# Optimization experiments

Measured on AMD Instinct MI355X. Metric: run time of the kernel, lower is better.

The kernel has to match this reference:

```python
import jax, jax.numpy as jnp
import numpy as np

KERNEL_SIZE = 3  # init kwarg
METRIC = 'MSE'   # init kwarg


def setup_inputs() -> dict:
    key = jax.random.key(0)
    k1, k2, k3 = jax.random.split(key, 3)
    B, H, W, S = 16, 2048, 2048, 5000
    predictions = jax.random.normal(k1, (B, 1, H, W), dtype=jnp.float32)
    # pos[...,0] = px in [0,W), pos[...,1] = py in [0,H)
    station_positions = jax.random.randint(k2, (B, S, 2), 0, 2048, dtype=jnp.int32)
    station_runoffs = jax.random.normal(k3, (B, S), dtype=jnp.float32)
    return {
        'predictions': predictions,
        'station_positions': station_positions,
        'station_runoffs': station_runoffs,
    }


def reference(predictions, station_positions, station_runoffs):
    B, _, H, W = predictions.shape
    kh = KERNEL_SIZE // 2
    # kernel offsets, flattened to (K2,)
    offs = jnp.arange(-kh, kh + 1)
    dy, dx = jnp.meshgrid(offs, offs, indexing='ij')
    dy = dy.reshape(-1)
    dx = dx.reshape(-1)
    px = station_positions[..., 0]  # (B,S) -> width index
    py = station_positions[..., 1]  # (B,S) -> height index
    ys = py[..., None] + dy  # (B,S,K2)
    xs = px[..., None] + dx  # (B,S,K2)
    valid = (ys >= 0) & (ys < H) & (xs >= 0) & (xs < W)
    ysc = jnp.clip(ys, 0, H - 1)
    xsc = jnp.clip(xs, 0, W - 1)
    b_idx = jnp.arange(B)[:, None, None]
    vals = predictions[b_idx, 0, ysc, xsc]  # (B,S,K2) gathered neighborhoods
    validf = valid.astype(predictions.dtype)
    counts = validf.sum(-1)  # >=4 always (corner of 3x3 window)
    avg_pred = (vals * validf).sum(-1) / counts  # (B,S) per-station window mean
    if METRIC == 'MSE':
        per_station = (avg_pred - station_runoffs) ** 2
    else:  # MAE
        per_station = jnp.abs(avg_pred - station_runoffs)
    # original: sum of per-station losses / num_stations
    return jnp.mean(per_station)
```

## Files before the change

### kernel.cpp

```cpp
#include <hip/hip_runtime.h>


#define BB 16
#define HH 2048
#define WW 2048
#define SS 5000
#define NSTATIONS (BB * SS)

__global__ __launch_bounds__(256) void station_loss_kernel(
    const float* __restrict__ pred,
    const int2*  __restrict__ pos,
    const float* __restrict__ runoff,
    float* __restrict__ out)
{
    int t = blockIdx.x * blockDim.x + threadIdx.x;
    float contrib = 0.0f;
    if (t < NSTATIONS) {
        int b = t / SS;
        int2 p = pos[t];
        int px = p.x;
        int py = p.y;
        const float* img = pred + (size_t)b * (size_t)HH * (size_t)WW;

        float sum = 0.0f;
        float cnt = 0.0f;
        #pragma unroll
        for (int dy = -1; dy <= 1; ++dy) {
            int y = py + dy;
            if (y < 0 || y >= HH) continue;
            const float* row = img + (size_t)y * WW;
            #pragma unroll
            for (int dx = -1; dx <= 1; ++dx) {
                int x = px + dx;
                if (x < 0 || x >= WW) continue;
                sum += row[x];
                cnt += 1.0f;
            }
        }
        float avg = sum / cnt;
        float d = avg - runoff[t];
        contrib = d * d * (1.0f / (float)NSTATIONS);
    }

    #pragma unroll
    for (int off = 32; off > 0; off >>= 1)
        contrib += __shfl_down(contrib, off, 64);

    if ((threadIdx.x & 63) == 0)
        atomicAdd(out, contrib);
}

extern "C" void kernel_launch(void* const* d_in, const int* in_sizes, int n_in,
                              void* d_out, int out_size, void* d_ws, size_t ws_size,
                              hipStream_t stream) {
    const float* pred   = (const float*)d_in[0];
    const int2*  pos    = (const int2*)d_in[1];
    const float* runoff = (const float*)d_in[2];
    float* out = (float*)d_out;

    hipMemsetAsync(out, 0, sizeof(float), stream);

    const int threads = 256;
    const int blocks = (NSTATIONS + threads - 1) / threads;
    station_loss_kernel<<<blocks, threads, 0, stream>>>(pred, pos, runoff, out);
}
```

Measured before the change: 319.4 us.

## Replace global atomics with two-stage block-partial reduction and branchless gathers

Each block now reduces its station losses through shared memory and writes one partial to workspace. A single-block second kernel sums the partials and applies the mean scaling, which replaces the memset and per-wave atomicAdd. The window gathers now use clamped indices and masks instead of branches, so all nine loads are issued unconditionally. The cost is an extra kernel launch and a reliance on the workspace buffer.

```diff
diff --git a/kernel.cpp b/kernel.cpp
--- a/kernel.cpp
+++ b/kernel.cpp
@@ -6,12 +6,14 @@
 #define WW 2048
 #define SS 5000
 #define NSTATIONS (BB * SS)
+#define THREADS 256
+#define NBLOCKS ((NSTATIONS + THREADS - 1) / THREADS)
 
-__global__ __launch_bounds__(256) void station_loss_kernel(
+__global__ __launch_bounds__(THREADS) void station_partial_kernel(
     const float* __restrict__ pred,
     const int2*  __restrict__ pos,
     const float* __restrict__ runoff,
-    float* __restrict__ out)
+    float* __restrict__ partials)
 {
     int t = blockIdx.x * blockDim.x + threadIdx.x;
     float contrib = 0.0f;
@@ -20,34 +22,69 @@
         int2 p = pos[t];
         int px = p.x;
         int py = p.y;
-        const float* img = pred + (size_t)b * (size_t)HH * (size_t)WW;
+        const float* img = pred + (size_t)b * (size_t)(HH * WW);
 
         float sum = 0.0f;
         float cnt = 0.0f;
         #pragma unroll
         for (int dy = -1; dy <= 1; ++dy) {
             int y = py + dy;
-            if (y < 0 || y >= HH) continue;
-            const float* row = img + (size_t)y * WW;
+            bool yok = (y >= 0) & (y < HH);
+            int yc = min(max(y, 0), HH - 1);
+            const float* row = img + (size_t)yc * WW;
             #pragma unroll
             for (int dx = -1; dx <= 1; ++dx) {
                 int x = px + dx;
-                if (x < 0 || x >= WW) continue;
-                sum += row[x];
-                cnt += 1.0f;
+                bool ok = yok & (x >= 0) & (x < WW);
+                int xc = min(max(x, 0), WW - 1);
+                float v = row[xc];
+                float m = ok ? 1.0f : 0.0f;
+                sum += v * m;
+                cnt += m;
             }
         }
         float avg = sum / cnt;
         float d = avg - runoff[t];
-        contrib = d * d * (1.0f / (float)NSTATIONS);
+        contrib = d * d;
     }
 
     #pragma unroll
     for (int off = 32; off > 0; off >>= 1)
         contrib += __shfl_down(contrib, off, 64);
 
-    if ((threadIdx.x & 63) == 0)
-        atomicAdd(out, contrib);
+    __shared__ float waves[THREADS / 64];
+    int lane = threadIdx.x & 63;
+    int wid  = threadIdx.x >> 6;
+    if (lane == 0) waves[wid] = contrib;
+    __syncthreads();
+    if (threadIdx.x == 0) {
+        float s = 0.0f;
+        #pragma unroll
+        for (int i = 0; i < THREADS / 64; ++i) s += waves[i];
+        partials[blockIdx.x] = s;
+    }
+}
+
+__global__ __launch_bounds__(512) void reduce_kernel(
+    const float* __restrict__ partials, float* __restrict__ out)
+{
+    float v = 0.0f;
+    for (int i = threadIdx.x; i < NBLOCKS; i += 512) v += partials[i];
+    #pragma unroll
+    for (int off = 32; off > 0; off >>= 1)
+        v += __shfl_down(v, off, 64);
+
+    __shared__ float waves[512 / 64];
+    int lane = threadIdx.x & 63;
+    int wid  = threadIdx.x >> 6;
+    if (lane == 0) waves[wid] = v;
+    __syncthreads();
+    if (threadIdx.x == 0) {
+        float s = 0.0f;
+        #pragma unroll
+        for (int i = 0; i < 512 / 64; ++i) s += waves[i];
+        out[0] = s * (1.0f / (float)NSTATIONS);
+    }
 }
 
 extern "C" void kernel_launch(void* const* d_in, const int* in_sizes, int n_in,
@@ -56,11 +93,9 @@
     const float* pred   = (const float*)d_in[0];
     const int2*  pos    = (const int2*)d_in[1];
     const float* runoff = (const float*)d_in[2];
-    float* out = (float*)d_out;
+    float* out      = (float*)d_out;
+    float* partials = (float*)d_ws;
 
-    hipMemsetAsync(out, 0, sizeof(float), stream);
-
-    const int threads = 256;
-    const int blocks = (NSTATIONS + threads - 1) / threads;
-    station_loss_kernel<<<blocks, threads, 0, stream>>>(pred, pos, runoff, out);
+    station_partial_kernel<<<NBLOCKS, THREADS, 0, stream>>>(pred, pos, runoff, partials);
+    reduce_kernel<<<1, 512, 0, stream>>>(partials, out);
 }
```

Result: faster. 308.5 us (-3.4%).
